# Optimization experiments

Hardware: AMD Instinct MI355X
Metric: run time of the kernel (lower is better)

Reference implementation:

```python
import jax, jax.numpy as jnp
import numpy as np


def setup_inputs() -> dict:
    key = jax.random.key(0)
    kx, kq, kk, kv = jax.random.split(key, 4)
    B, S, D_IN, H, D_OUT = 2, 2048, 768, 12, 64
    scale = 0.02
    return {
        "x": jax.random.normal(kx, (B, S, D_IN), dtype=jnp.float32),
        "Wq": jax.random.normal(kq, (H, D_IN, D_OUT), dtype=jnp.float32) * scale,
        "Wk": jax.random.normal(kk, (H, D_IN, D_OUT), dtype=jnp.float32) * scale,
        "Wv": jax.random.normal(kv, (H, D_IN, D_OUT), dtype=jnp.float32) * scale,
    }


def reference(x, Wq, Wk, Wv):
    # x: [B, S, d_in]; Wq/Wk/Wv: [H, d_in, d_out] (stacked per-head Linear weights, no bias)
    B, S, _ = x.shape
    H, _, d_out = Wq.shape
    q = jnp.einsum("bsd,hde->bhse", x, Wq)  # [B, H, S, d_out]
    k = jnp.einsum("bsd,hde->bhse", x, Wk)
    v = jnp.einsum("bsd,hde->bhse", x, Wv)
    scores = jnp.einsum("bhse,bhte->bhst", q, k) / jnp.sqrt(jnp.float32(d_out))
    causal = jnp.tril(jnp.ones((S, S), dtype=bool))  # True = keep
    scores = jnp.where(causal, scores, jnp.float32(-jnp.inf))
    attn = jax.nn.softmax(scores, axis=-1)  # dropout = 0.0 -> identity
    ctx = jnp.einsum("bhst,bhte->bhse", attn, v)  # [B, H, S, d_out]
    # concat heads along last dim: [B, S, H*d_out]
    return ctx.transpose(0, 2, 1, 3).reshape(B, S, H * d_out)
```

## Files before the change

### kernel.cpp

```cpp
#include <hip/hip_runtime.h>
#include <hip/hip_bf16.h>


typedef short bf16x8 __attribute__((ext_vector_type(8)));
typedef short bf16x4 __attribute__((ext_vector_type(4)));
typedef float f32x4  __attribute__((ext_vector_type(4)));

#define MFMA16(a, b, c)  __builtin_amdgcn_mfma_f32_16x16x32_bf16((a), (b), (c), 0, 0, 0)
#define MFMAK16(a, b, c) __builtin_amdgcn_mfma_f32_16x16x16bf16_1k((a), (b), (c), 0, 0, 0)

static __device__ __forceinline__ unsigned short f2bf(float f) {
    unsigned int u = __builtin_bit_cast(unsigned int, f);
    u += 0x7fffu + ((u >> 16) & 1u);
    return (unsigned short)(u >> 16);
}

static __device__ __forceinline__ int sw(int row, int cb) {
    return (row << 7) + (cb ^ ((row & 7) << 4));
}

static __device__ __forceinline__ void gld16(const void* g, void* l) {
    __builtin_amdgcn_global_load_lds(
        (__attribute__((address_space(1))) void*)g,
        (__attribute__((address_space(3))) void*)l, 16, 0, 0);
}

__global__ __launch_bounds__(256) void prep(const float* __restrict__ x,
                                            const float* __restrict__ Wq,
                                            const float* __restrict__ Wk,
                                            const float* __restrict__ Wv,
                                            char* __restrict__ xb,
                                            char* __restrict__ wtb) {
    __shared__ float tile[64][65];
    const int bid = blockIdx.x;
    const int t = threadIdx.x;
    if (bid < 768) {
        const int stile = bid & 63, ks = bid >> 6;
        const int row = t >> 2, k16 = (t & 3) * 16;
        const float* src = x + (size_t)(stile * 64 + row) * 768 + ks * 64 + k16;
        char* img = xb + ((size_t)stile * 12 + ks) * 8192;
        const float4 v0 = *(const float4*)(src);
        const float4 v1 = *(const float4*)(src + 4);
        const float4 v2 = *(const float4*)(src + 8);
        const float4 v3 = *(const float4*)(src + 12);
        bf16x8 o0, o1;
        o0[0] = (short)f2bf(v0.x); o0[1] = (short)f2bf(v0.y);
        o0[2] = (short)f2bf(v0.z); o0[3] = (short)f2bf(v0.w);
        o0[4] = (short)f2bf(v1.x); o0[5] = (short)f2bf(v1.y);
        o0[6] = (short)f2bf(v1.z); o0[7] = (short)f2bf(v1.w);
        o1[0] = (short)f2bf(v2.x); o1[1] = (short)f2bf(v2.y);
        o1[2] = (short)f2bf(v2.z); o1[3] = (short)f2bf(v2.w);
        o1[4] = (short)f2bf(v3.x); o1[5] = (short)f2bf(v3.y);
        o1[6] = (short)f2bf(v3.z); o1[7] = (short)f2bf(v3.w);
        *(bf16x8*)(img + sw(row, k16 * 2)) = o0;
        *(bf16x8*)(img + sw(row, k16 * 2 + 16)) = o1;
    } else {
        const int idx = bid - 768;
        const int wh = idx % 36, dt = idx / 36;
        const int w = wh / 12, h = wh % 12;
        const float* W = (w == 0) ? Wq : (w == 1) ? Wk : Wv;
        for (int i = 0; i < 4; ++i) {
            int c = t + i * 256;
            int d = c >> 4, e4 = (c & 15) * 4;
            const float4 v = *(const float4*)(W + (size_t)(h * 768 + dt * 64 + d) * 64 + e4);
            tile[d][e4 + 0] = v.x; tile[d][e4 + 1] = v.y;
            tile[d][e4 + 2] = v.z; tile[d][e4 + 3] = v.w;
        }
        __syncthreads();
        char* img = wtb + ((size_t)(wh * 12) + dt) * 8192;
        for (int i = 0; i < 4; ++i) {
            int c = t + i * 256;
            int e = c >> 4, d4 = (c & 15) * 4;
            ushort4 o;
            o.x = f2bf(tile[d4 + 0][e]); o.y = f2bf(tile[d4 + 1][e]);
            o.z = f2bf(tile[d4 + 2][e]); o.w = f2bf(tile[d4 + 3][e]);
            *(ushort4*)(img + e * 128 + ((d4 * 2) ^ ((e & 7) << 4))) = o;
        }
    }
}

__global__ __launch_bounds__(256) void proj_qkv(const char* __restrict__ xb,
                                                const char* __restrict__ wtb,
                                                unsigned short* __restrict__ q,
                                                unsigned short* __restrict__ ksw,
                                                char* __restrict__ vsw) {
    __shared__ __align__(16) char smem[65536];
    const int stile = blockIdx.x;
    const int h = blockIdx.y;
    const int t = threadIdx.x;
    const int wave = t >> 6, lane = t & 63;
    const int lhi = lane >> 4, llo = lane & 15;
    const int wr = wave >> 1, wc = wave & 1;

    const char* asrc = xb + (size_t)stile * 12 * 8192;

    f32x4 acc[3][2][2] = {};

    #define STAGE(KS, BUF)                                                       \
        do {                                                                     \
            const char* s0 = asrc + (KS) * 8192;                                 \
            char* d0 = smem + (BUF) * 32768;                                     \
            gld16(s0 + t * 16, d0 + t * 16);                                     \
            gld16(s0 + t * 16 + 4096, d0 + t * 16 + 4096);                       \
            for (int w3 = 0; w3 < 3; ++w3) {                                     \
                const char* s1 = wtb + ((size_t)((w3 * 12 + h) * 12) + (KS)) * 8192; \
                char* d1 = smem + (BUF) * 32768 + (1 + w3) * 8192;               \
                gld16(s1 + t * 16, d1 + t * 16);                                 \
                gld16(s1 + t * 16 + 4096, d1 + t * 16 + 4096);                   \
            }                                                                    \
        } while (0)

    STAGE(0, 0);
    __syncthreads();
    int cur = 0;
    for (int ks = 0; ks < 12; ++ks) {
        if (ks < 11) STAGE(ks + 1, cur ^ 1);
        char* Alds = smem + cur * 32768;
        #pragma unroll
        for (int kk = 0; kk < 2; ++kk) {
            bf16x8 a[2];
            #pragma unroll
            for (int m = 0; m < 2; ++m)
                a[m] = *(const bf16x8*)(Alds + sw(wr * 32 + m * 16 + llo, kk * 64 + lhi * 16));
            #pragma unroll
            for (int w3 = 0; w3 < 3; ++w3) {
                char* Blds = Alds + (1 + w3) * 8192;
                #pragma unroll
                for (int n = 0; n < 2; ++n) {
                    bf16x8 b = *(const bf16x8*)(Blds + sw(wc * 32 + n * 16 + llo, kk * 64 + lhi * 16));
                    #pragma unroll
                    for (int m = 0; m < 2; ++m)
                        acc[w3][m][n] = MFMA16(a[m], b, acc[w3][m][n]);
                }
            }
        }
        __syncthreads();
        cur ^= 1;
    }
    #undef STAGE

    const float SCALE_Q = 0.18033688011112042f;
    const int bglob = stile >> 5, ktile = stile & 31;
    const int bh = bglob * 12 + h;
    #pragma unroll
    for (int m = 0; m < 2; ++m)
        for (int n = 0; n < 2; ++n)
            for (int r = 0; r < 4; ++r) {
                int s = (stile * 64 + wr * 32 + m * 16 + lhi * 4 + r) & 2047;
                int e = wc * 32 + n * 16 + llo;
                q[(size_t)(bh * 2048 + s) * 64 + e] = f2bf(acc[0][m][n][r] * SCALE_Q);
            }
    unsigned short* kdst = ksw + ((size_t)bh * 32 + ktile) * 4096;
    #pragma unroll
    for (int m = 0; m < 2; ++m)
        for (int n = 0; n < 2; ++n)
            for (int r = 0; r < 4; ++r) {
                int kk = wr * 32 + m * 16 + lhi * 4 + r;
                int e = wc * 32 + n * 16 + llo;
                kdst[kk * 64 + (e ^ ((kk & 7) << 3))] = f2bf(acc[1][m][n][r]);
            }
    char* vtimg = smem;
    __syncthreads();
    #pragma unroll
    for (int m = 0; m < 2; ++m)
        for (int n = 0; n < 2; ++n)
            for (int r = 0; r < 4; ++r) {
                int kk = wr * 32 + m * 16 + lhi * 4 + r;
                int e = wc * 32 + n * 16 + llo;
                int pos = (((kk >> 2) & 3) * 32 + (kk >> 4) * 8 + (kk & 3) * 2) ^ ((e & 7) << 4);
                *(unsigned short*)(vtimg + e * 128 + pos) = f2bf(acc[2][m][n][r]);
            }
    __syncthreads();
    {
        char* dst = vsw + ((size_t)bh * 32 + ktile) * 8192;
        #pragma unroll
        for (int i = 0; i < 2; ++i)
            *(float4*)(dst + t * 16 + i * 4096) =
                *(const float4*)(vtimg + t * 16 + i * 4096);
    }
}

__global__ __launch_bounds__(256) void attn(const unsigned short* __restrict__ Q,
                                            const char* __restrict__ Ksw,
                                            const char* __restrict__ Vsw,
                                            float* __restrict__ out) {
    __shared__ __align__(16) char smem[32768];
    const int t = threadIdx.x, wave = t >> 6, lane = t & 63;
    const int lhi = lane >> 4, llo = lane & 15;
    const int bid = blockIdx.x;
    const int tt = bid & 31, grp = (bid >> 5) & 7, e3 = bid >> 8;
    const int qt = (e3 == 0) ? tt
                 : (e3 == 1) ? ((tt + 16) & 31)
                             : ((tt < 16) ? 30 - 2 * tt : 63 - 2 * tt);
    const int bh = grp * 3 + e3;
    const unsigned short* Qg = Q + (size_t)bh * 2048 * 64;
    const char* Kg = Ksw + (size_t)bh * 32 * 8192;
    const char* Vg = Vsw + (size_t)bh * 32 * 8192;

    const int q0 = qt * 64 + wave * 16;
    bf16x8 qa[2];
    #pragma unroll
    for (int kk = 0; kk < 2; ++kk)
        qa[kk] = *(const bf16x8*)(Qg + (size_t)(q0 + llo) * 64 + kk * 32 + lhi * 8);

    f32x4 acc[4] = {};
    float m_r = -1e30f, l_r = 0.f;

    #define ASTAGE(KT, BUF)                                              \
        do {                                                             \
            const char* ks_ = Kg + (size_t)(KT) * 8192;                  \
            const char* vs_ = Vg + (size_t)(KT) * 8192;                  \
            char* kd = smem + (BUF) * 8192;                              \
            char* vd = smem + 16384 + (BUF) * 8192;                      \
            gld16(ks_ + t * 16, kd + t * 16);                            \
            gld16(ks_ + t * 16 + 4096, kd + t * 16 + 4096);              \
            gld16(vs_ + t * 16, vd + t * 16);                            \
            gld16(vs_ + t * 16 + 4096, vd + t * 16 + 4096);              \
        } while (0)

    ASTAGE(0, 0);
    __syncthreads();
    int cur = 0;
    for (int kt = 0; kt <= qt; ++kt) {
        if (kt < qt) ASTAGE(kt + 1, cur ^ 1);
        char* Kb = smem + cur * 8192;
        char* Vb = smem + 16384 + cur * 8192;

        f32x4 sc[4];
        __builtin_amdgcn_s_setprio(1);
        #pragma unroll
        for (int n = 0; n < 4; ++n) {
            f32x4 z = {};
            #pragma unroll
            for (int kk = 0; kk < 2; ++kk) {
                bf16x8 bk = *(const bf16x8*)(Kb + sw(n * 16 + llo, kk * 64 + lhi * 16));
                z = MFMA16(bk, qa[kk], z);
            }
            sc[n] = z;
        }
        __builtin_amdgcn_s_setprio(0);
        bf16x8 vfr[4][2];
        #pragma unroll
        for (int n = 0; n < 4; ++n) {
            const int row = n * 16 + llo;
            vfr[n][0] = *(const bf16x8*)(Vb + sw(row, lhi * 32));
            vfr[n][1] = *(const bf16x8*)(Vb + sw(row, lhi * 32 + 16));
        }
        if (kt == qt) {
            #pragma unroll
            for (int n = 0; n < 4; ++n)
                #pragma unroll
                for (int r = 0; r < 4; ++r)
                    if (kt * 64 + n * 16 + lhi * 4 + r > q0 + llo) sc[n][r] = -1e30f;
        }
        float pmax = fmaxf(
            fmaxf(fmaxf(fmaxf(sc[0][0], sc[0][1]), fmaxf(sc[0][2], sc[0][3])),
                  fmaxf(fmaxf(sc[1][0], sc[1][1]), fmaxf(sc[1][2], sc[1][3]))),
            fmaxf(fmaxf(fmaxf(sc[2][0], sc[2][1]), fmaxf(sc[2][2], sc[2][3])),
                  fmaxf(fmaxf(sc[3][0], sc[3][1]), fmaxf(sc[3][2], sc[3][3]))));
        if (__any(pmax > m_r + 8.0f)) {
            float tm = fmaxf(pmax, __shfl_xor(pmax, 16, 64));
            tm = fmaxf(tm, __shfl_xor(tm, 32, 64));
            float nm = fmaxf(m_r, tm);
            float corr = exp2f(m_r - nm);
            m_r = nm;
            l_r *= corr;
            #pragma unroll
            for (int n = 0; n < 4; ++n)
                #pragma unroll
                for (int r = 0; r < 4; ++r) acc[n][r] *= corr;
        }
        bf16x4 pf[4];
        float ps = 0.f;
        #pragma unroll
        for (int kb = 0; kb < 4; ++kb) {
            float p0 = exp2f(sc[kb][0] - m_r), p1 = exp2f(sc[kb][1] - m_r);
            float p2 = exp2f(sc[kb][2] - m_r), p3 = exp2f(sc[kb][3] - m_r);
            ps += (p0 + p1) + (p2 + p3);
            unsigned int w0, w1;
            asm("v_cvt_pk_bf16_f32 %0, %1, %2" : "=v"(w0) : "v"(p0), "v"(p1));
            asm("v_cvt_pk_bf16_f32 %0, %1, %2" : "=v"(w1) : "v"(p2), "v"(p3));
            unsigned long long u = ((unsigned long long)w1 << 32) | w0;
            pf[kb] = __builtin_bit_cast(bf16x4, u);
        }
        l_r += ps;
        __builtin_amdgcn_s_setprio(1);
        #pragma unroll
        for (int n = 0; n < 4; ++n) {
            f32x4 a = acc[n];
            a = MFMAK16(__builtin_shufflevector(vfr[n][0], vfr[n][0], 0, 1, 2, 3), pf[0], a);
            a = MFMAK16(__builtin_shufflevector(vfr[n][0], vfr[n][0], 4, 5, 6, 7), pf[1], a);
            a = MFMAK16(__builtin_shufflevector(vfr[n][1], vfr[n][1], 0, 1, 2, 3), pf[2], a);
            a = MFMAK16(__builtin_shufflevector(vfr[n][1], vfr[n][1], 4, 5, 6, 7), pf[3], a);
            acc[n] = a;
        }
        __builtin_amdgcn_s_setprio(0);
        if (kt < qt) __syncthreads();
        cur ^= 1;
    }
    #undef ASTAGE
    l_r += __shfl_xor(l_r, 16, 64);
    l_r += __shfl_xor(l_r, 32, 64);
    const float inv = 1.0f / l_r;
    const int b = bh / 12, h = bh - b * 12;
    #pragma unroll
    for (int n = 0; n < 4; ++n) {
        float4 o;
        o.x = acc[n][0] * inv; o.y = acc[n][1] * inv;
        o.z = acc[n][2] * inv; o.w = acc[n][3] * inv;
        *(float4*)(out + (size_t)(b * 2048 + q0 + llo) * 768 + h * 64 + n * 16 + lhi * 4) = o;
    }
}

extern "C" void kernel_launch(void* const* d_in, const int* in_sizes, int n_in,
                              void* d_out, int out_size, void* d_ws, size_t ws_size,
                              hipStream_t stream) {
    const float* x  = (const float*)d_in[0];
    const float* Wq = (const float*)d_in[1];
    const float* Wk = (const float*)d_in[2];
    const float* Wv = (const float*)d_in[3];
    float* out = (float*)d_out;

    char* ws = (char*)d_ws;
    char*           wtb = ws;
    unsigned short* q   = (unsigned short*)(ws + 3538944);
    unsigned short* ksw = (unsigned short*)(ws + 9830400);
    char*           vsw = (char*)(ws + 16121856);
    char*           xb  = (char*)(ws + 22413312);

    hipLaunchKernelGGL(prep, dim3(1200), dim3(256), 0, stream, x, Wq, Wk, Wv, xb, wtb);
    hipLaunchKernelGGL(proj_qkv, dim3(64, 12), dim3(256), 0, stream,
                       xb, wtb, q, ksw, vsw);
    hipLaunchKernelGGL(attn, dim3(768), dim3(256), 0, stream, q, (const char*)ksw, vsw, out);
}
```

Baseline: 70.46 us.

## Split long causal query tiles across two blocks and merge with a combine kernel

Query tiles 16-31 are split along the key dimension into two halves, each computed by its own block. Each half writes unnormalized partial outputs plus running max and sum to a workspace buffer, and a new combine kernel merges them with log-sum-exp weights. Work is assigned by a snake-ordered rank scheme so blocks of similar cost land in the same wave of dispatch. The aim is to shorten the longest per-block critical path and balance load across CUs. The cost is an extra kernel launch and extra global traffic for the partial results.

```diff
diff --git a/kernel.cpp b/kernel.cpp
--- a/kernel.cpp
+++ b/kernel.cpp
@@ -183,16 +183,30 @@
 __global__ __launch_bounds__(256) void attn(const unsigned short* __restrict__ Q,
                                             const char* __restrict__ Ksw,
                                             const char* __restrict__ Vsw,
-                                            float* __restrict__ out) {
+                                            float* __restrict__ out,
+                                            float* __restrict__ Obuf,
+                                            float* __restrict__ mlbuf) {
     __shared__ __align__(16) char smem[32768];
     const int t = threadIdx.x, wave = t >> 6, lane = t & 63;
     const int lhi = lane >> 4, llo = lane & 15;
-    const int bid = blockIdx.x;
-    const int tt = bid & 31, grp = (bid >> 5) & 7, e3 = bid >> 8;
-    const int qt = (e3 == 0) ? tt
-                 : (e3 == 1) ? ((tt + 16) & 31)
-                             : ((tt < 16) ? 30 - 2 * tt : 63 - 2 * tt);
-    const int bh = grp * 3 + e3;
+    const int round = blockIdx.x >> 8, pos = blockIdx.x & 255;
+    const int rank = (round & 1) ? (round << 8) + (255 - pos) : (int)blockIdx.x;
+    int bh, qt, kts, kte;
+    bool split; int part = 0;
+    if (rank < 432) {
+        bh = rank % 24;
+        const int j = rank / 24;
+        if (j < 16)      { qt = 16 + j; part = 0; kts = 0;  kte = 15; split = true;  }
+        else if (j == 16){ qt = 15;              kts = 0;  kte = 15; split = false; }
+        else             { qt = 31;     part = 1; kts = 16; kte = 31; split = true;  }
+    } else {
+        const int g = (rank - 432) / 48;
+        const int r2 = (rank - 432) % 48;
+        bh = r2 % 24;
+        const int s = 15 - g;
+        if (r2 / 24 == 0) { qt = s - 1;            kts = 0;  kte = qt; split = false; }
+        else              { qt = s + 15; part = 1; kts = 16; kte = qt; split = true;  }
+    }
     const unsigned short* Qg = Q + (size_t)bh * 2048 * 64;
     const char* Kg = Ksw + (size_t)bh * 32 * 8192;
     const char* Vg = Vsw + (size_t)bh * 32 * 8192;
@@ -218,11 +232,11 @@
             gld16(vs_ + t * 16 + 4096, vd + t * 16 + 4096);              \
         } while (0)
 
-    ASTAGE(0, 0);
+    ASTAGE(kts, 0);
     __syncthreads();
     int cur = 0;
-    for (int kt = 0; kt <= qt; ++kt) {
-        if (kt < qt) ASTAGE(kt + 1, cur ^ 1);
+    for (int kt = kts; kt <= kte; ++kt) {
+        if (kt < kte) ASTAGE(kt + 1, cur ^ 1);
         char* Kb = smem + cur * 8192;
         char* Vb = smem + 16384 + cur * 8192;
 
@@ -295,20 +309,66 @@
             acc[n] = a;
         }
         __builtin_amdgcn_s_setprio(0);
-        if (kt < qt) __syncthreads();
+        if (kt < kte) __syncthreads();
         cur ^= 1;
     }
     #undef ASTAGE
     l_r += __shfl_xor(l_r, 16, 64);
     l_r += __shfl_xor(l_r, 32, 64);
-    const float inv = 1.0f / l_r;
+    if (split) {
+        const int p = ((bh * 16) + (qt - 16)) * 2 + part;
+        float* Ob = Obuf + (size_t)p * 4096;
+        const int qrow = wave * 16 + llo;
+        #pragma unroll
+        for (int n = 0; n < 4; ++n) {
+            float4 o;
+            o.x = acc[n][0]; o.y = acc[n][1]; o.z = acc[n][2]; o.w = acc[n][3];
+            *(float4*)(Ob + qrow * 64 + n * 16 + lhi * 4) = o;
+        }
+        if (lhi == 0) {
+            float2 ml; ml.x = m_r; ml.y = l_r;
+            *(float2*)(mlbuf + (size_t)p * 128 + qrow * 2) = ml;
+        }
+    } else {
+        const float inv = 1.0f / l_r;
+        const int b = bh / 12, h = bh - b * 12;
+        #pragma unroll
+        for (int n = 0; n < 4; ++n) {
+            float4 o;
+            o.x = acc[n][0] * inv; o.y = acc[n][1] * inv;
+            o.z = acc[n][2] * inv; o.w = acc[n][3] * inv;
+            *(float4*)(out + (size_t)(b * 2048 + q0 + llo) * 768 + h * 64 + n * 16 + lhi * 4) = o;
+        }
+    }
+}
+
+__global__ __launch_bounds__(256) void combine(const float* __restrict__ Obuf,
+                                               const float* __restrict__ mlbuf,
+                                               float* __restrict__ out) {
+    const int bid = blockIdx.x;
+    const int bh = bid % 24, qt = 16 + bid / 24;
     const int b = bh / 12, h = bh - b * 12;
-    #pragma unroll
-    for (int n = 0; n < 4; ++n) {
+    const int t = threadIdx.x;
+    const int r = t >> 2, c0 = (t & 3) * 16;
+    const int p0 = ((bh * 16) + (qt - 16)) * 2;
+    const float2 ml0 = *(const float2*)(mlbuf + (size_t)p0 * 128 + r * 2);
+    const float2 ml1 = *(const float2*)(mlbuf + (size_t)(p0 + 1) * 128 + r * 2);
+    const float mm = fmaxf(ml0.x, ml1.x);
+    const float w0 = exp2f(ml0.x - mm), w1 = exp2f(ml1.x - mm);
+    const float inv = 1.0f / (ml0.y * w0 + ml1.y * w1);
+    const float* s0 = Obuf + (size_t)p0 * 4096 + r * 64 + c0;
+    const float* s1 = s0 + 4096;
+    float* dst = out + (size_t)(b * 2048 + qt * 64 + r) * 768 + h * 64 + c0;
+    #pragma unroll
+    for (int i = 0; i < 4; ++i) {
+        const float4 a = *(const float4*)(s0 + i * 4);
+        const float4 c = *(const float4*)(s1 + i * 4);
         float4 o;
-        o.x = acc[n][0] * inv; o.y = acc[n][1] * inv;
-        o.z = acc[n][2] * inv; o.w = acc[n][3] * inv;
-        *(float4*)(out + (size_t)(b * 2048 + q0 + llo) * 768 + h * 64 + n * 16 + lhi * 4) = o;
+        o.x = (a.x * w0 + c.x * w1) * inv;
+        o.y = (a.y * w0 + c.y * w1) * inv;
+        o.z = (a.z * w0 + c.z * w1) * inv;
+        o.w = (a.w * w0 + c.w * w1) * inv;
+        *(float4*)(dst + i * 4) = o;
     }
 }
 
@@ -322,14 +382,18 @@
     float* out = (float*)d_out;
 
     char* ws = (char*)d_ws;
-    char*           wtb = ws;
-    unsigned short* q   = (unsigned short*)(ws + 3538944);
-    unsigned short* ksw = (unsigned short*)(ws + 9830400);
-    char*           vsw = (char*)(ws + 16121856);
-    char*           xb  = (char*)(ws + 22413312);
+    char*           wtb   = ws;
+    unsigned short* q     = (unsigned short*)(ws + 3538944);
+    unsigned short* ksw   = (unsigned short*)(ws + 9830400);
+    char*           vsw   = (char*)(ws + 16121856);
+    char*           xb    = (char*)(ws + 22413312);
+    float*          Obuf  = (float*)(ws + 28704768);
+    float*          mlbuf = (float*)(ws + 41287680);
 
     hipLaunchKernelGGL(prep, dim3(1200), dim3(256), 0, stream, x, Wq, Wk, Wv, xb, wtb);
     hipLaunchKernelGGL(proj_qkv, dim3(64, 12), dim3(256), 0, stream,
                        xb, wtb, q, ksw, vsw);
-    hipLaunchKernelGGL(attn, dim3(768), dim3(256), 0, stream, q, (const char*)ksw, vsw, out);
-}
+    hipLaunchKernelGGL(attn, dim3(1152), dim3(256), 0, stream,
+                       q, (const char*)ksw, vsw, out, Obuf, mlbuf);
+    hipLaunchKernelGGL(combine, dim3(384), dim3(256), 0, stream, Obuf, mlbuf, out);
+}
```

Result: faster. 68.33 us (median of 2 runs) (-3.0%).
